# Kernel optimization log

Measured on AMD Instinct MI355X. Metric: run time of the kernel, lower is better.

The kernel has to match this reference:

```python
import jax, jax.numpy as jnp
from jax import lax
import numpy as np


def _conv3x3(x, w, b):
    # x: [B,C,H,W], w: [O,I,3,3] (OIHW), SAME padding, stride 1
    y = lax.conv_general_dilated(x, w, window_strides=(1, 1), padding='SAME',
                                 dimension_numbers=('NCHW', 'OIHW', 'NCHW'))
    return y + b[None, :, None, None]


def setup_inputs() -> dict:
    key = jax.random.key(0)
    ks = jax.random.split(key, 9)
    B, C, H, W = 4, 64, 64, 64
    wscale = 1.0 / np.sqrt(C * 9)  # keep conv outputs / attention logits sane
    x = jax.random.normal(ks[0], (B, C, H, W), dtype=jnp.float32)
    wq = jax.random.normal(ks[1], (C, C, 3, 3), dtype=jnp.float32) * wscale
    bq = jax.random.normal(ks[2], (C,), dtype=jnp.float32) * 0.1
    wk = jax.random.normal(ks[3], (C, C, 3, 3), dtype=jnp.float32) * wscale
    bk = jax.random.normal(ks[4], (C,), dtype=jnp.float32) * 0.1
    wv = jax.random.normal(ks[5], (C, C, 3, 3), dtype=jnp.float32) * wscale
    bv = jax.random.normal(ks[6], (C,), dtype=jnp.float32) * 0.1
    pos_gamma = jax.random.normal(ks[7], (1,), dtype=jnp.float32)
    chan_gamma = jax.random.normal(ks[8], (1,), dtype=jnp.float32)
    return {'x': x, 'wq': wq, 'bq': bq, 'wk': wk, 'bk': bk, 'wv': wv, 'bv': bv,
            'pos_gamma': pos_gamma, 'chan_gamma': chan_gamma}


def reference(x, wq, bq, wk, bk, wv, bv, pos_gamma, chan_gamma):
    B, C, H, W = x.shape
    N = H * W
    # position (spatial) self-attention over N = H*W locations
    q = _conv3x3(x, wq, bq).reshape(B, C, N)
    k = _conv3x3(x, wk, bk).reshape(B, C, N)
    v = _conv3x3(x, wv, bv).reshape(B, C, N)
    # attn[b,i,j] = softmax_j( sum_c q[b,c,i] * k[b,c,j] )
    pos_attn = jax.nn.softmax(jnp.einsum('bci,bcj->bij', q, k), axis=-1)
    # pos_out[b,c,j] = sum_i v[b,c,i] * attn[b,i,j]  (matches torch.bmm(v, attn))
    pos = jnp.einsum('bci,bij->bcj', v, pos_attn).reshape(B, C, H, W)
    pos_out = pos_gamma * pos + x
    # channel self-attention over C channels (x is its own q/k/v)
    xf = x.reshape(B, C, N)
    chan_attn = jax.nn.softmax(jnp.einsum('bcn,bdn->bcd', xf, xf), axis=-1)
    chan = jnp.einsum('bcd,bdn->bcn', chan_attn, xf).reshape(B, C, H, W)
    chan_out = chan_gamma * chan + x
    return pos_out + chan_out
```

## Files before the change

### kernel.cpp

```cpp
#include <hip/hip_runtime.h>

#define OFF_XV2   65536u
#define OFF_GP    589824u
#define OFF_Q2    1048576u
#define OFF_K2    2097152u
#define OFF_V2    3145728u
#define OFF_X2    3670016u
#define OFF_WT    4194304u
#define OFF_INVL  4452352u
#define OFF_A     4730880u
#define WS_FLOATS 4747264u

typedef short s8v __attribute__((ext_vector_type(8)));
typedef float f16v __attribute__((ext_vector_type(16)));

#define MFMA32(a, b, c) __builtin_amdgcn_mfma_f32_32x32x16_bf16((a), (b), (c), 0, 0, 0)

__device__ __forceinline__ unsigned short bf16_rne(float f) {
    union { float f; unsigned int u; } v; v.f = f;
    unsigned int r = v.u + 0x7FFFu + ((v.u >> 16) & 1u);
    return (unsigned short)(r >> 16);
}
__device__ __forceinline__ float bf2f(unsigned short h) {
    union { unsigned int u; float f; } t; t.u = ((unsigned int)h) << 16;
    return t.f;
}
__device__ __forceinline__ void split2(float f, unsigned short& h, unsigned short& l) {
    unsigned short hh = bf16_rne(f);
    h = hh;
    l = bf16_rne(f - bf2f(hh));
}
__device__ __forceinline__ unsigned int cvtpk(float lo, float hi) {
    unsigned int r;
    asm("v_cvt_pk_bf16_f32 %0, %1, %2" : "=v"(r) : "v"(lo), "v"(hi));
    return r;
}
__device__ __forceinline__ void pl32swap(unsigned int& a, unsigned int& b) {
    asm volatile("v_permlane32_swap_b32 %0, %1" : "+v"(a), "+v"(b));
}
__device__ __forceinline__ s8v mk8(unsigned int w0, unsigned int w1,
                                   unsigned int w2, unsigned int w3) {
    union { unsigned int u[4]; s8v v; } t;
    t.u[0] = w0; t.u[1] = w1; t.u[2] = w2; t.u[3] = w3;
    return t.v;
}
__device__ __forceinline__ f16v zero16() {
    f16v z;
#pragma unroll
    for (int i = 0; i < 16; ++i) z[i] = 0.0f;
    return z;
}


__global__ void k_wtrans(const float* __restrict__ wq, const float* __restrict__ wk,
                         const float* __restrict__ wv, unsigned short* __restrict__ wf) {
    int t = blockIdx.x * 256 + threadIdx.x;
    int f = t >> 9, pos = t & 511;
    int lane = pos >> 3, e = pos & 7;
    int oc = f & 1, kst = (f >> 1) & 3;
    int ct = f >> 3;
    int tap = ct % 9, conv = ct / 9;
    int o = oc * 32 + (lane & 31);
    int ci = kst * 16 + (lane >> 5) * 8 + e;
    const float* w = (conv == 0) ? wq : (conv == 1) ? wk : wv;
    float v = w[(o * 64 + ci) * 9 + tap];
    unsigned short hh, ll;
    split2(v, hh, ll);
    wf[(f * 2 + 0) * 512 + pos] = hh;
    wf[(f * 2 + 1) * 512 + pos] = ll;
}

__global__ __launch_bounds__(256) void k_xpack(const float* __restrict__ x,
                                               unsigned short* __restrict__ X2,
                                               unsigned short* __restrict__ XV2) {
    int gid = blockIdx.x * 256 + threadIdx.x;
    int b = gid >> 16;
    int c = (gid >> 10) & 63;
    int n4 = (gid & 1023) * 4;
    float4 v = *(const float4*)(x + (size_t)(b * 64 + c) * 4096 + n4);
    unsigned short hv[4] = {bf16_rne(v.x), bf16_rne(v.y), bf16_rne(v.z), bf16_rne(v.w)};
    int kst = c >> 4, e = c & 7, hb = (c >> 3) & 1;
#pragma unroll
    for (int u = 0; u < 4; ++u) {
        int n = n4 + u;
        int nch = n >> 5, lane = (n & 31) + 32 * hb;
        X2[(size_t)((b * 128 + nch) * 4 + kst) * 512 + lane * 8 + e] = hv[u];
    }
    int ich = n4 >> 5, ksub = (n4 >> 4) & 1, cb = c >> 5;
    int lane2 = (c & 31) + 32 * ((n4 >> 3) & 1);
    size_t xi = (size_t)(((b * 128 + ich) * 2 + ksub) * 2 + cb) * 512 + lane2 * 8 + (n4 & 7);
    unsigned long long w = (unsigned long long)hv[0]
                         | ((unsigned long long)hv[1] << 16)
                         | ((unsigned long long)hv[2] << 32)
                         | ((unsigned long long)hv[3] << 48);
    *(unsigned long long*)(XV2 + xi) = w;
}

__global__ __launch_bounds__(384) void k_conv(
        const float* __restrict__ x, const unsigned short* __restrict__ wf,
        const float* __restrict__ bq, const float* __restrict__ bk, const float* __restrict__ bv,
        unsigned short* __restrict__ Q2, unsigned short* __restrict__ K2,
        unsigned short* __restrict__ V2) {
    int nb = blockIdx.x;
    int b = blockIdx.y;
    int h = nb >> 1, w0 = (nb & 1) * 32;

    __shared__ unsigned short xwh[6528];
    __shared__ unsigned short xwl[6528];

    int tid = threadIdx.x;
    for (int idx = tid; idx < 6528; idx += 384) {
        int W = idx % 34;
        int c = (idx / 34) & 63;
        int dy = idx / (34 * 64);
        int hs = h + dy - 1, wi = w0 + W - 1;
        float v = 0.0f;
        if (hs >= 0 && hs < 64 && wi >= 0 && wi < 64)
            v = x[((b * 64 + c) * 64 + hs) * 64 + wi];
        unsigned short hh_, ll_;
        split2(v, hh_, ll_);
        int row = dy * 34 + W;
        int byt = row * 128 + c * 2;
        int swz = byt ^ ((row & 7) << 4);
        *(unsigned short*)((char*)xwh + swz) = hh_;
        *(unsigned short*)((char*)xwl + swz) = ll_;
    }
    __syncthreads();

    int lane = tid & 63, wv = tid >> 6;
    int conv = wv >> 1, oc = wv & 1;
    int hh = lane >> 5, l31 = lane & 31;

    const float* bias = (conv == 0) ? bq : (conv == 1) ? bk : bv;
    f16v D;
    if (conv < 2) {
#pragma unroll
        for (int r = 0; r < 16; ++r)
            D[r] = bias[oc * 32 + (r & 3) + 8 * (r >> 2) + 4 * hh];
    } else {
        float bvv = bias[oc * 32 + l31];
#pragma unroll
        for (int r = 0; r < 16; ++r) D[r] = bvv;
    }

#pragma unroll
    for (int tap = 0; tap < 9; ++tap) {
        int dy = tap / 3, dx = tap % 3;
#pragma unroll
        for (int kst = 0; kst < 4; ++kst) {
            int f = ((conv * 9 + tap) * 4 + kst) * 2 + oc;
            s8v Wh = *(const s8v*)(wf + (f * 2 + 0) * 512 + lane * 8);
            s8v Wl = *(const s8v*)(wf + (f * 2 + 1) * 512 + lane * 8);
            int row = dy * 34 + dx + l31;
            int byt = row * 128 + kst * 32 + hh * 16;
            int swz = byt ^ ((row & 7) << 4);
            s8v Xh = *(const s8v*)((const char*)xwh + swz);
            s8v Xl = *(const s8v*)((const char*)xwl + swz);
            if (conv < 2) {
                D = MFMA32(Wh, Xh, D);
                D = MFMA32(Wh, Xl, D);
                D = MFMA32(Wl, Xh, D);
            } else {
                D = MFMA32(Xh, Wh, D);
                D = MFMA32(Xl, Wh, D);
                D = MFMA32(Xh, Wl, D);
            }
        }
    }

    if (conv < 2) {
        unsigned short sh[16], sl[16];
#pragma unroll
        for (int r = 0; r < 16; ++r) split2(D[r], sh[r], sl[r]);
        unsigned int ah0 = sh[0] | ((unsigned int)sh[1] << 16), ah1 = sh[2] | ((unsigned int)sh[3] << 16);
        unsigned int ah2 = sh[4] | ((unsigned int)sh[5] << 16), ah3 = sh[6] | ((unsigned int)sh[7] << 16);
        pl32swap(ah0, ah2); pl32swap(ah1, ah3);
        s8v F0h = mk8(ah0, ah1, ah2, ah3);
        unsigned int al0 = sl[0] | ((unsigned int)sl[1] << 16), al1 = sl[2] | ((unsigned int)sl[3] << 16);
        unsigned int al2 = sl[4] | ((unsigned int)sl[5] << 16), al3 = sl[6] | ((unsigned int)sl[7] << 16);
        pl32swap(al0, al2); pl32swap(al1, al3);
        s8v F0l = mk8(al0, al1, al2, al3);
        unsigned int bh0 = sh[8] | ((unsigned int)sh[9] << 16), bh1 = sh[10] | ((unsigned int)sh[11] << 16);
        unsigned int bh2 = sh[12] | ((unsigned int)sh[13] << 16), bh3 = sh[14] | ((unsigned int)sh[15] << 16);
        pl32swap(bh0, bh2); pl32swap(bh1, bh3);
        s8v F1h = mk8(bh0, bh1, bh2, bh3);
        unsigned int bl0 = sl[8] | ((unsigned int)sl[9] << 16), bl1 = sl[10] | ((unsigned int)sl[11] << 16);
        unsigned int bl2 = sl[12] | ((unsigned int)sl[13] << 16), bl3 = sl[14] | ((unsigned int)sl[15] << 16);
        pl32swap(bl0, bl2); pl32swap(bl1, bl3);
        s8v F1l = mk8(bl0, bl1, bl2, bl3);
        unsigned short* dst = (conv == 0) ? Q2 : K2;
        size_t b0 = (size_t)(((b * 128 + nb) * 4 + oc * 2 + 0) * 2) * 512 + lane * 8;
        size_t b1 = (size_t)(((b * 128 + nb) * 4 + oc * 2 + 1) * 2) * 512 + lane * 8;
        *(s8v*)(dst + b0) = F0h;
        *(s8v*)(dst + b0 + 512) = F0l;
        *(s8v*)(dst + b1) = F1h;
        *(s8v*)(dst + b1 + 512) = F1l;
    } else {
        unsigned int a0 = cvtpk(D[0], D[1]),  a1 = cvtpk(D[2], D[3]);
        unsigned int a2 = cvtpk(D[4], D[5]),  a3 = cvtpk(D[6], D[7]);
        pl32swap(a0, a2); pl32swap(a1, a3);
        s8v F0h = mk8(a0, a1, a2, a3);
        unsigned int b0w = cvtpk(D[8], D[9]),  b1w = cvtpk(D[10], D[11]);
        unsigned int b2w = cvtpk(D[12], D[13]), b3w = cvtpk(D[14], D[15]);
        pl32swap(b0w, b2w); pl32swap(b1w, b3w);
        s8v F1h = mk8(b0w, b1w, b2w, b3w);
        size_t v0 = (size_t)(((b * 128 + nb) * 2 + 0) * 2 + oc) * 512 + lane * 8;
        size_t v1 = (size_t)(((b * 128 + nb) * 2 + 1) * 2 + oc) * 512 + lane * 8;
        *(s8v*)(V2 + v0) = F0h;
        *(s8v*)(V2 + v1) = F1h;
    }
}

__global__ __launch_bounds__(256) void k_gram(const unsigned short* __restrict__ XV2,
                                              float* __restrict__ Gp) {
    int kp = blockIdx.x, b = blockIdx.y;
    int tid = threadIdx.x, lane = tid & 63, wv = tid >> 6;
    int cb1 = wv & 1, cb2 = wv >> 1;
    f16v G = zero16();
#pragma unroll
    for (int t = 0; t < 8; ++t) {
        int ich = kp * 8 + t;
        const unsigned short* base = XV2 + (size_t)(b * 128 + ich) * 2048 + lane * 8;
        s8v a0 = *(const s8v*)(base + (0 * 2 + cb1) * 512);
        s8v b0 = *(const s8v*)(base + (0 * 2 + cb2) * 512);
        s8v a1 = *(const s8v*)(base + (1 * 2 + cb1) * 512);
        s8v b1 = *(const s8v*)(base + (1 * 2 + cb2) * 512);
        G = MFMA32(a0, b0, G);
        G = MFMA32(a1, b1, G);
    }
    int hh = lane >> 5, l31 = lane & 31;
#pragma unroll
    for (int r = 0; r < 16; ++r) {
        int cc = cb1 * 32 + (r & 3) + 8 * (r >> 2) + 4 * hh;
        int dd = cb2 * 32 + l31;
        Gp[(size_t)(kp * 4 + b) * 4096 + cc * 64 + dd] = G[r];
    }
}

__global__ void k_asm(const float* __restrict__ Gp, unsigned short* __restrict__ A2) {
    int row = blockIdx.x;
    int d = threadIdx.x;
    int b = row >> 6, c = row & 63;
    float g = 0.0f;
#pragma unroll
    for (int p = 0; p < 16; ++p) g += Gp[(size_t)(p * 4 + b) * 4096 + c * 64 + d];
    float mx = g;
    for (int off = 32; off >= 1; off >>= 1) mx = fmaxf(mx, __shfl_xor(mx, off, 64));
    float e = __expf(g - mx);
    float s = e;
    for (int off = 32; off >= 1; off >>= 1) s += __shfl_xor(s, off, 64);
    float a = e / s;
    int cb = c >> 5, kst = d >> 4;
    int lane2 = (c & 31) + 32 * ((d >> 3) & 1);
    A2[(size_t)((b * 2 + cb) * 4 + kst) * 512 + lane2 * 8 + (d & 7)] = bf16_rne(a);
}

__global__ __launch_bounds__(512, 2) void k_pass1(
        const unsigned short* __restrict__ Q2, const unsigned short* __restrict__ K2,
        float* __restrict__ invl) {
    int flat = blockIdx.x;
    int xcd = flat & 7;
    int b = xcd >> 1;
    int ichp = (xcd & 1) * 32 + (flat >> 3);
    int ich0 = ichp * 2;
    int tid = threadIdx.x, lane = tid & 63, wv = tid >> 6;

    __shared__ float lsum[8][2][32];

    const unsigned short* qp = Q2 + (size_t)(b * 128 + ich0) * 4096 + lane * 8;
    s8v q0f0 = *(const s8v*)(qp);
    s8v q0f1 = *(const s8v*)(qp + 512);
    s8v q0f2 = *(const s8v*)(qp + 1024);
    s8v q0f3 = *(const s8v*)(qp + 1536);
    s8v q0f4 = *(const s8v*)(qp + 2048);
    s8v q0f5 = *(const s8v*)(qp + 2560);
    s8v q0f6 = *(const s8v*)(qp + 3072);
    s8v q0f7 = *(const s8v*)(qp + 3584);
    s8v q1f0 = *(const s8v*)(qp + 4096);
    s8v q1f1 = *(const s8v*)(qp + 4608);
    s8v q1f2 = *(const s8v*)(qp + 5120);
    s8v q1f3 = *(const s8v*)(qp + 5632);
    s8v q1f4 = *(const s8v*)(qp + 6144);
    s8v q1f5 = *(const s8v*)(qp + 6656);
    s8v q1f6 = *(const s8v*)(qp + 7168);
    s8v q1f7 = *(const s8v*)(qp + 7680);

    float la0 = 0.f, la1 = 0.f, lb0 = 0.f, lb1 = 0.f;
#pragma unroll 1
    for (int t = 0; t < 16; ++t) {
        int jch = wv * 16 + t;
        const unsigned short* kp = K2 + (size_t)(b * 128 + jch) * 4096 + lane * 8;
        s8v kf0 = *(const s8v*)(kp);
        s8v kf1 = *(const s8v*)(kp + 512);
        s8v kf2 = *(const s8v*)(kp + 1024);
        s8v kf3 = *(const s8v*)(kp + 1536);
        s8v kf4 = *(const s8v*)(kp + 2048);
        s8v kf5 = *(const s8v*)(kp + 2560);
        s8v kf6 = *(const s8v*)(kp + 3072);
        s8v kf7 = *(const s8v*)(kp + 3584);
        {
            f16v Sa = zero16(), Sb = zero16();
            Sa = MFMA32(kf0, q0f0, Sa);
            Sa = MFMA32(kf0, q0f1, Sa);
            Sa = MFMA32(kf1, q0f0, Sa);
            Sa = MFMA32(kf2, q0f2, Sa);
            Sa = MFMA32(kf2, q0f3, Sa);
            Sa = MFMA32(kf3, q0f2, Sa);
            Sb = MFMA32(kf4, q0f4, Sb);
            Sb = MFMA32(kf4, q0f5, Sb);
            Sb = MFMA32(kf5, q0f4, Sb);
            Sb = MFMA32(kf6, q0f6, Sb);
            Sb = MFMA32(kf6, q0f7, Sb);
            Sb = MFMA32(kf7, q0f6, Sb);
#pragma unroll
            for (int r = 0; r < 8; ++r) la0 += __expf(Sa[r] + Sb[r]);
#pragma unroll
            for (int r = 8; r < 16; ++r) la1 += __expf(Sa[r] + Sb[r]);
        }
        {
            f16v Sa = zero16(), Sb = zero16();
            Sa = MFMA32(kf0, q1f0, Sa);
            Sa = MFMA32(kf0, q1f1, Sa);
            Sa = MFMA32(kf1, q1f0, Sa);
            Sa = MFMA32(kf2, q1f2, Sa);
            Sa = MFMA32(kf2, q1f3, Sa);
            Sa = MFMA32(kf3, q1f2, Sa);
            Sb = MFMA32(kf4, q1f4, Sb);
            Sb = MFMA32(kf4, q1f5, Sb);
            Sb = MFMA32(kf5, q1f4, Sb);
            Sb = MFMA32(kf6, q1f6, Sb);
            Sb = MFMA32(kf6, q1f7, Sb);
            Sb = MFMA32(kf7, q1f6, Sb);
#pragma unroll
            for (int r = 0; r < 8; ++r) lb0 += __expf(Sa[r] + Sb[r]);
#pragma unroll
            for (int r = 8; r < 16; ++r) lb1 += __expf(Sa[r] + Sb[r]);
        }
    }
    float lacc0 = la0 + la1;
    lacc0 += __shfl_xor(lacc0, 32);
    float lacc1 = lb0 + lb1;
    lacc1 += __shfl_xor(lacc1, 32);
    if (lane < 32) {
        lsum[wv][0][lane] = lacc0;
        lsum[wv][1][lane] = lacc1;
    }
    __syncthreads();
    if (tid < 64) {
        int ic = tid >> 5, iL = tid & 31;
        float s = 0.f;
#pragma unroll
        for (int p = 0; p < 8; ++p) s += lsum[p][ic][iL];
        invl[b * 4096 + (ich0 + ic) * 32 + iL] = 1.0f / s;
    }
}

__global__ __launch_bounds__(256) void k_vnorm(
        unsigned short* __restrict__ V2, const float* __restrict__ invl) {
    int u = blockIdx.x * 256 + threadIdx.x;
    int lane = u & 63, ksub = (u >> 7) & 1;
    int ich = (u >> 8) & 127, b = u >> 15;
    int n0 = ich * 32 + ksub * 16 + (lane >> 5) * 8;
    size_t base = (size_t)u * 8;
    s8v vh = *(s8v*)(V2 + base);
    float4 iv0 = *(const float4*)(invl + b * 4096 + n0);
    float4 iv1 = *(const float4*)(invl + b * 4096 + n0 + 4);
    float ivv[8] = {iv0.x, iv0.y, iv0.z, iv0.w, iv1.x, iv1.y, iv1.z, iv1.w};
    s8v o;
#pragma unroll
    for (int e = 0; e < 8; ++e)
        o[e] = (short)bf16_rne(bf2f((unsigned short)vh[e]) * ivv[e]);
    *(s8v*)(V2 + base) = o;
}

__global__ __launch_bounds__(512, 2) void k_pass2(
        const unsigned short* __restrict__ Q2, const unsigned short* __restrict__ K2,
        const unsigned short* __restrict__ V2, const unsigned short* __restrict__ X2,
        const unsigned short* __restrict__ A2, const float* __restrict__ x,
        const float* __restrict__ pg, const float* __restrict__ cg,
        float* __restrict__ out) {
    int flat = blockIdx.x;
    int xcd = flat & 7;
    int b = xcd >> 1;
    int jtp = (xcd & 1) * 32 + (flat >> 3);
    int jt0 = jtp * 2;
    int tid = threadIdx.x, lane = tid & 63, wv = tid >> 6;

    __shared__ float smem[12288];
    unsigned short* Klds = (unsigned short*)(smem + 8192);
    float* rl = smem;

    {
        const unsigned short* ksrc = K2 + (size_t)(b * 128 + jt0) * 4096;
#pragma unroll
        for (int s = 0; s < 2; ++s) {
            int seg = tid + s * 512;
            *(s8v*)(Klds + seg * 8) = *(const s8v*)(ksrc + seg * 8);
        }
    }
    __syncthreads();

    f16v O0a = zero16(), O1a = zero16();
    f16v O0b = zero16(), O1b = zero16();

#pragma unroll 1
    for (int t = 0; t < 16; ++t) {
        int ich = wv * 16 + t;
        const unsigned short* qp = Q2 + (size_t)(b * 128 + ich) * 4096 + lane * 8;
        s8v qf0 = *(const s8v*)(qp);
        s8v qf1 = *(const s8v*)(qp + 512);
        s8v qf2 = *(const s8v*)(qp + 1024);
        s8v qf3 = *(const s8v*)(qp + 1536);
        s8v qf4 = *(const s8v*)(qp + 2048);
        s8v qf5 = *(const s8v*)(qp + 2560);
        s8v qf6 = *(const s8v*)(qp + 3072);
        s8v qf7 = *(const s8v*)(qp + 3584);
        const unsigned short* vp = V2 + (size_t)(b * 128 + ich) * 2048 + lane * 8;
        s8v vA = *(const s8v*)(vp);
        s8v vB = *(const s8v*)(vp + 512);
        s8v vC = *(const s8v*)(vp + 1024);
        s8v vD = *(const s8v*)(vp + 1536);

#pragma unroll
        for (int js = 0; js < 2; ++js) {
            const unsigned short* kl = Klds + js * 4096 + lane * 8;
            s8v kf0 = *(const s8v*)(kl);
            s8v kf1 = *(const s8v*)(kl + 512);
            s8v kf2 = *(const s8v*)(kl + 1024);
            s8v kf3 = *(const s8v*)(kl + 1536);
            s8v kf4 = *(const s8v*)(kl + 2048);
            s8v kf5 = *(const s8v*)(kl + 2560);
            s8v kf6 = *(const s8v*)(kl + 3072);
            s8v kf7 = *(const s8v*)(kl + 3584);

            f16v Sa = zero16(), Sb = zero16();
            Sa = MFMA32(qf0, kf0, Sa);
            Sa = MFMA32(qf0, kf1, Sa);
            Sa = MFMA32(qf1, kf0, Sa);
            Sa = MFMA32(qf2, kf2, Sa);
            Sa = MFMA32(qf2, kf3, Sa);
            Sa = MFMA32(qf3, kf2, Sa);
            Sb = MFMA32(qf4, kf4, Sb);
            Sb = MFMA32(qf4, kf5, Sb);
            Sb = MFMA32(qf5, kf4, Sb);
            Sb = MFMA32(qf6, kf6, Sb);
            Sb = MFMA32(qf6, kf7, Sb);
            Sb = MFMA32(qf7, kf6, Sb);

            float p[16];
#pragma unroll
            for (int r = 0; r < 16; ++r) p[r] = __expf(Sa[r] + Sb[r]);

            unsigned int a0 = cvtpk(p[0], p[1]),  a1 = cvtpk(p[2], p[3]);
            unsigned int a2 = cvtpk(p[4], p[5]),  a3 = cvtpk(p[6], p[7]);
            pl32swap(a0, a2);
            pl32swap(a1, a3);
            s8v P0 = mk8(a0, a1, a2, a3);
            unsigned int b0 = cvtpk(p[8], p[9]),  b1 = cvtpk(p[10], p[11]);
            unsigned int b2 = cvtpk(p[12], p[13]), b3 = cvtpk(p[14], p[15]);
            pl32swap(b0, b2);
            pl32swap(b1, b3);
            s8v P1 = mk8(b0, b1, b2, b3);

            if (js == 0) {
                O0a = MFMA32(vA, P0, O0a);
                O0a = MFMA32(vC, P1, O0a);
                O1a = MFMA32(vB, P0, O1a);
                O1a = MFMA32(vD, P1, O1a);
            } else {
                O0b = MFMA32(vA, P0, O0b);
                O0b = MFMA32(vC, P1, O0b);
                O1b = MFMA32(vB, P0, O1b);
                O1b = MFMA32(vD, P1, O1b);
            }
        }
    }

    int hh = lane >> 5, jj = lane & 31;
    float s0[4], s1[4];
    if (wv < 4) {
#pragma unroll
        for (int r = 0; r < 16; ++r) {
            int c = (r & 3) + 8 * (r >> 2) + 4 * hh;
            rl[(wv * 64 + c) * 32 + jj] = O0a[r];
            rl[(wv * 64 + c + 32) * 32 + jj] = O1a[r];
        }
    }
    __syncthreads();
#pragma unroll
    for (int k = 0; k < 4; ++k) {
        int el = tid + k * 512;
        s0[k] = ((rl[el] + rl[2048 + el]) + rl[4096 + el]) + rl[6144 + el];
    }
    __syncthreads();
    if (wv >= 4) {
#pragma unroll
        for (int r = 0; r < 16; ++r) {
            int c = (r & 3) + 8 * (r >> 2) + 4 * hh;
            rl[((wv - 4) * 64 + c) * 32 + jj] = O0a[r];
            rl[((wv - 4) * 64 + c + 32) * 32 + jj] = O1a[r];
        }
    }
    __syncthreads();
#pragma unroll
    for (int k = 0; k < 4; ++k) {
        int el = tid + k * 512;
        s0[k] = ((s0[k] + rl[el]) + rl[2048 + el]) + rl[4096 + el];
        s0[k] += rl[6144 + el];
    }
    __syncthreads();
    if (wv < 4) {
#pragma unroll
        for (int r = 0; r < 16; ++r) {
            int c = (r & 3) + 8 * (r >> 2) + 4 * hh;
            rl[(wv * 64 + c) * 32 + jj] = O0b[r];
            rl[(wv * 64 + c + 32) * 32 + jj] = O1b[r];
        }
    }
    __syncthreads();
#pragma unroll
    for (int k = 0; k < 4; ++k) {
        int el = tid + k * 512;
        s1[k] = ((rl[el] + rl[2048 + el]) + rl[4096 + el]) + rl[6144 + el];
    }
    __syncthreads();
    if (wv >= 4) {
#pragma unroll
        for (int r = 0; r < 16; ++r) {
            int c = (r & 3) + 8 * (r >> 2) + 4 * hh;
            rl[((wv - 4) * 64 + c) * 32 + jj] = O0b[r];
            rl[((wv - 4) * 64 + c + 32) * 32 + jj] = O1b[r];
        }
    }
    __syncthreads();
#pragma unroll
    for (int k = 0; k < 4; ++k) {
        int el = tid + k * 512;
        s1[k] = ((s1[k] + rl[el]) + rl[2048 + el]) + rl[4096 + el];
        s1[k] += rl[6144 + el];
    }
    __syncthreads();

    float* chan = smem;
    float* xres = smem + 4160;
    if (wv < 4) {
        int jts = wv >> 1, cb = wv & 1;
        f16v Dc = zero16();
#pragma unroll
        for (int kst = 0; kst < 4; ++kst) {
            s8v af = *(const s8v*)(A2 + (size_t)((b * 2 + cb) * 4 + kst) * 512 + lane * 8);
            s8v xf = *(const s8v*)(X2 + (size_t)((b * 128 + jt0 + jts) * 4 + kst) * 512 + lane * 8);
            Dc = MFMA32(af, xf, Dc);
        }
#pragma unroll
        for (int r = 0; r < 16; ++r) {
            int c = cb * 32 + (r & 3) + 8 * (r >> 2) + 4 * hh;
            chan[c * 65 + jts * 32 + jj] = Dc[r];
        }
    }
#pragma unroll
    for (int k = 0; k < 8; ++k) {
        int el = tid + k * 512;
        int c = el >> 6, j2 = el & 63;
        xres[el] = x[(size_t)(b * 64 + c) * 4096 + jtp * 64 + j2];
    }
    __syncthreads();
    float pgv = pg[0], cgv = cg[0];
#pragma unroll
    for (int k = 0; k < 4; ++k) {
        int el = tid + k * 512;
        int c = el >> 5, j2 = el & 31;
        size_t ob = (size_t)(b * 64 + c) * 4096 + jtp * 64;
        out[ob + j2] = pgv * s0[k] + cgv * chan[c * 65 + j2] + 2.0f * xres[c * 64 + j2];
        out[ob + 32 + j2] = pgv * s1[k] + cgv * chan[c * 65 + 32 + j2] + 2.0f * xres[c * 64 + 32 + j2];
    }
}

extern "C" void kernel_launch(void* const* d_in, const int* in_sizes, int n_in,
                              void* d_out, int out_size, void* d_ws, size_t ws_size,
                              hipStream_t stream) {
    const float* x  = (const float*)d_in[0];
    const float* wq = (const float*)d_in[1];
    const float* bq = (const float*)d_in[2];
    const float* wk = (const float*)d_in[3];
    const float* bk = (const float*)d_in[4];
    const float* wv = (const float*)d_in[5];
    const float* bv = (const float*)d_in[6];
    const float* pg = (const float*)d_in[7];
    const float* cg = (const float*)d_in[8];
    float* out = (float*)d_out;

    if (ws_size < (size_t)WS_FLOATS * sizeof(float)) return;
    float* ws = (float*)d_ws;
    unsigned short* XV2 = (unsigned short*)(ws + OFF_XV2);
    float* Gp = ws + OFF_GP;
    unsigned short* Q2  = (unsigned short*)(ws + OFF_Q2);
    unsigned short* K2  = (unsigned short*)(ws + OFF_K2);
    unsigned short* V2  = (unsigned short*)(ws + OFF_V2);
    unsigned short* X2  = (unsigned short*)(ws + OFF_X2);
    unsigned short* wfb = (unsigned short*)(ws + OFF_WT);
    float* invl = ws + OFF_INVL;
    unsigned short* A2  = (unsigned short*)(ws + OFF_A);

    k_wtrans<<<432, 256, 0, stream>>>(wq, wk, wv, wfb);
    k_xpack<<<1024, 256, 0, stream>>>(x, X2, XV2);
    k_conv<<<dim3(128, 4), 384, 0, stream>>>(x, wfb, bq, bk, bv, Q2, K2, V2);
    k_gram<<<dim3(16, 4), 256, 0, stream>>>(XV2, Gp);
    k_asm<<<256, 64, 0, stream>>>(Gp, A2);
    k_pass1<<<256, 512, 0, stream>>>(Q2, K2, invl);
    k_vnorm<<<512, 256, 0, stream>>>(V2, invl);
    k_pass2<<<256, 512, 0, stream>>>(Q2, K2, V2, X2, A2, x, pg, cg, out);
}
```

Baseline: 110.2 us.

## Split attention passes over key/query halves and move epilogue to final kernel

The two attention passes now split the reduction dimension in half, launching twice as many blocks (512) so more CUs are occupied. Partial row sums and partial outputs go to workspace and are combined in the normalization kernel and in a new final kernel, which also does the channel-attention MFMA and the residual. The two small prep kernels are merged into one launch. In exchange there is extra global traffic for the partial results and one more kernel launch.

```diff
diff --git a/kernel.cpp b/kernel.cpp
--- a/kernel.cpp
+++ b/kernel.cpp
@@ -1,5 +1,7 @@
 #include <hip/hip_runtime.h>
 
+#define OFF_LP    0u
+#define OFF_OP1   0u
 #define OFF_XV2   65536u
 #define OFF_GP    589824u
 #define OFF_Q2    1048576u
@@ -7,7 +9,6 @@
 #define OFF_V2    3145728u
 #define OFF_X2    3670016u
 #define OFF_WT    4194304u
-#define OFF_INVL  4452352u
 #define OFF_A     4730880u
 #define WS_FLOATS 4747264u
 
@@ -52,48 +53,50 @@
 }
 
 
-__global__ void k_wtrans(const float* __restrict__ wq, const float* __restrict__ wk,
-                         const float* __restrict__ wv, unsigned short* __restrict__ wf) {
-    int t = blockIdx.x * 256 + threadIdx.x;
-    int f = t >> 9, pos = t & 511;
-    int lane = pos >> 3, e = pos & 7;
-    int oc = f & 1, kst = (f >> 1) & 3;
-    int ct = f >> 3;
-    int tap = ct % 9, conv = ct / 9;
-    int o = oc * 32 + (lane & 31);
-    int ci = kst * 16 + (lane >> 5) * 8 + e;
-    const float* w = (conv == 0) ? wq : (conv == 1) ? wk : wv;
-    float v = w[(o * 64 + ci) * 9 + tap];
-    unsigned short hh, ll;
-    split2(v, hh, ll);
-    wf[(f * 2 + 0) * 512 + pos] = hh;
-    wf[(f * 2 + 1) * 512 + pos] = ll;
-}
-
-__global__ __launch_bounds__(256) void k_xpack(const float* __restrict__ x,
-                                               unsigned short* __restrict__ X2,
-                                               unsigned short* __restrict__ XV2) {
-    int gid = blockIdx.x * 256 + threadIdx.x;
-    int b = gid >> 16;
-    int c = (gid >> 10) & 63;
-    int n4 = (gid & 1023) * 4;
-    float4 v = *(const float4*)(x + (size_t)(b * 64 + c) * 4096 + n4);
-    unsigned short hv[4] = {bf16_rne(v.x), bf16_rne(v.y), bf16_rne(v.z), bf16_rne(v.w)};
-    int kst = c >> 4, e = c & 7, hb = (c >> 3) & 1;
-#pragma unroll
-    for (int u = 0; u < 4; ++u) {
-        int n = n4 + u;
-        int nch = n >> 5, lane = (n & 31) + 32 * hb;
-        X2[(size_t)((b * 128 + nch) * 4 + kst) * 512 + lane * 8 + e] = hv[u];
-    }
-    int ich = n4 >> 5, ksub = (n4 >> 4) & 1, cb = c >> 5;
-    int lane2 = (c & 31) + 32 * ((n4 >> 3) & 1);
-    size_t xi = (size_t)(((b * 128 + ich) * 2 + ksub) * 2 + cb) * 512 + lane2 * 8 + (n4 & 7);
-    unsigned long long w = (unsigned long long)hv[0]
-                         | ((unsigned long long)hv[1] << 16)
-                         | ((unsigned long long)hv[2] << 32)
-                         | ((unsigned long long)hv[3] << 48);
-    *(unsigned long long*)(XV2 + xi) = w;
+__global__ __launch_bounds__(256) void k_prep(
+        const float* __restrict__ wq, const float* __restrict__ wk,
+        const float* __restrict__ wv, const float* __restrict__ x,
+        unsigned short* __restrict__ wf, unsigned short* __restrict__ X2,
+        unsigned short* __restrict__ XV2) {
+    int bid = blockIdx.x, tid = threadIdx.x;
+    if (bid < 432) {
+        int t = bid * 256 + tid;
+        int f = t >> 9, pos = t & 511;
+        int lane = pos >> 3, e = pos & 7;
+        int oc = f & 1, kst = (f >> 1) & 3;
+        int ct = f >> 3;
+        int tap = ct % 9, conv = ct / 9;
+        int o = oc * 32 + (lane & 31);
+        int ci = kst * 16 + (lane >> 5) * 8 + e;
+        const float* w = (conv == 0) ? wq : (conv == 1) ? wk : wv;
+        float v = w[(o * 64 + ci) * 9 + tap];
+        unsigned short hh, ll;
+        split2(v, hh, ll);
+        wf[(f * 2 + 0) * 512 + pos] = hh;
+        wf[(f * 2 + 1) * 512 + pos] = ll;
+    } else {
+        int gid = (bid - 432) * 256 + tid;
+        int b = gid >> 16;
+        int c = (gid >> 10) & 63;
+        int n4 = (gid & 1023) * 4;
+        float4 v = *(const float4*)(x + (size_t)(b * 64 + c) * 4096 + n4);
+        unsigned short hv[4] = {bf16_rne(v.x), bf16_rne(v.y), bf16_rne(v.z), bf16_rne(v.w)};
+        int kst = c >> 4, e = c & 7, hb = (c >> 3) & 1;
+#pragma unroll
+        for (int u = 0; u < 4; ++u) {
+            int n = n4 + u;
+            int nch = n >> 5, lane = (n & 31) + 32 * hb;
+            X2[(size_t)((b * 128 + nch) * 4 + kst) * 512 + lane * 8 + e] = hv[u];
+        }
+        int ich = n4 >> 5, ksub = (n4 >> 4) & 1, cb = c >> 5;
+        int lane2 = (c & 31) + 32 * ((n4 >> 3) & 1);
+        size_t xi = (size_t)(((b * 128 + ich) * 2 + ksub) * 2 + cb) * 512 + lane2 * 8 + (n4 & 7);
+        unsigned long long w = (unsigned long long)hv[0]
+                             | ((unsigned long long)hv[1] << 16)
+                             | ((unsigned long long)hv[2] << 32)
+                             | ((unsigned long long)hv[3] << 48);
+        *(unsigned long long*)(XV2 + xi) = w;
+    }
 }
 
 __global__ __launch_bounds__(384) void k_conv(
@@ -257,11 +260,12 @@
 
 __global__ __launch_bounds__(512, 2) void k_pass1(
         const unsigned short* __restrict__ Q2, const unsigned short* __restrict__ K2,
-        float* __restrict__ invl) {
+        float* __restrict__ lpart) {
     int flat = blockIdx.x;
     int xcd = flat & 7;
     int b = xcd >> 1;
-    int ichp = (xcd & 1) * 32 + (flat >> 3);
+    int rest = (xcd & 1) * 64 + (flat >> 3);
+    int ichp = rest & 63, jh = rest >> 6;
     int ich0 = ichp * 2;
     int tid = threadIdx.x, lane = tid & 63, wv = tid >> 6;
 
@@ -287,8 +291,8 @@
 
     float la0 = 0.f, la1 = 0.f, lb0 = 0.f, lb1 = 0.f;
 #pragma unroll 1
-    for (int t = 0; t < 16; ++t) {
-        int jch = wv * 16 + t;
+    for (int t = 0; t < 8; ++t) {
+        int jch = jh * 64 + wv * 8 + t;
         const unsigned short* kp = K2 + (size_t)(b * 128 + jch) * 4096 + lane * 8;
         s8v kf0 = *(const s8v*)(kp);
         s8v kf1 = *(const s8v*)(kp + 512);
@@ -351,38 +355,43 @@
         float s = 0.f;
 #pragma unroll
         for (int p = 0; p < 8; ++p) s += lsum[p][ic][iL];
-        invl[b * 4096 + (ich0 + ic) * 32 + iL] = 1.0f / s;
-    }
-}
-
-__global__ __launch_bounds__(256) void k_vnorm(
-        unsigned short* __restrict__ V2, const float* __restrict__ invl) {
+        lpart[jh * 16384 + b * 4096 + (ich0 + ic) * 32 + iL] = s;
+    }
+}
+
+__global__ __launch_bounds__(256) void k_mvn(
+        unsigned short* __restrict__ V2, const float* __restrict__ lpart) {
     int u = blockIdx.x * 256 + threadIdx.x;
     int lane = u & 63, ksub = (u >> 7) & 1;
     int ich = (u >> 8) & 127, b = u >> 15;
     int n0 = ich * 32 + ksub * 16 + (lane >> 5) * 8;
     size_t base = (size_t)u * 8;
     s8v vh = *(s8v*)(V2 + base);
-    float4 iv0 = *(const float4*)(invl + b * 4096 + n0);
-    float4 iv1 = *(const float4*)(invl + b * 4096 + n0 + 4);
-    float ivv[8] = {iv0.x, iv0.y, iv0.z, iv0.w, iv1.x, iv1.y, iv1.z, iv1.w};
+    const float* l0 = lpart + b * 4096 + n0;
+    float4 a0 = *(const float4*)(l0);
+    float4 a1 = *(const float4*)(l0 + 4);
+    float4 c0 = *(const float4*)(l0 + 16384);
+    float4 c1 = *(const float4*)(l0 + 16384 + 4);
+    float lv[8] = {a0.x + c0.x, a0.y + c0.y, a0.z + c0.z, a0.w + c0.w,
+                   a1.x + c1.x, a1.y + c1.y, a1.z + c1.z, a1.w + c1.w};
     s8v o;
 #pragma unroll
-    for (int e = 0; e < 8; ++e)
-        o[e] = (short)bf16_rne(bf2f((unsigned short)vh[e]) * ivv[e]);
+    for (int e = 0; e < 8; ++e) {
+        float inv = 1.0f / lv[e];
+        o[e] = (short)bf16_rne(bf2f((unsigned short)vh[e]) * inv);
+    }
     *(s8v*)(V2 + base) = o;
 }
 
 __global__ __launch_bounds__(512, 2) void k_pass2(
         const unsigned short* __restrict__ Q2, const unsigned short* __restrict__ K2,
-        const unsigned short* __restrict__ V2, const unsigned short* __restrict__ X2,
-        const unsigned short* __restrict__ A2, const float* __restrict__ x,
-        const float* __restrict__ pg, const float* __restrict__ cg,
-        float* __restrict__ out) {
+        const unsigned short* __restrict__ V2, float* __restrict__ outp,
+        float* __restrict__ op1) {
     int flat = blockIdx.x;
     int xcd = flat & 7;
     int b = xcd >> 1;
-    int jtp = (xcd & 1) * 32 + (flat >> 3);
+    int rest = (xcd & 1) * 64 + (flat >> 3);
+    int jtp = rest & 63, ih = rest >> 6;
     int jt0 = jtp * 2;
     int tid = threadIdx.x, lane = tid & 63, wv = tid >> 6;
 
@@ -404,8 +413,8 @@
     f16v O0b = zero16(), O1b = zero16();
 
 #pragma unroll 1
-    for (int t = 0; t < 16; ++t) {
-        int ich = wv * 16 + t;
+    for (int t = 0; t < 8; ++t) {
+        int ich = ih * 64 + wv * 8 + t;
         const unsigned short* qp = Q2 + (size_t)(b * 128 + ich) * 4096 + lane * 8;
         s8v qf0 = *(const s8v*)(qp);
         s8v qf1 = *(const s8v*)(qp + 512);
@@ -539,11 +548,34 @@
         s1[k] = ((s1[k] + rl[el]) + rl[2048 + el]) + rl[4096 + el];
         s1[k] += rl[6144 + el];
     }
-    __syncthreads();
-
-    float* chan = smem;
-    float* xres = smem + 4160;
-    if (wv < 4) {
+
+    float* dst = ih ? op1 : outp;
+#pragma unroll
+    for (int k = 0; k < 4; ++k) {
+        int el = tid + k * 512;
+        int c = el >> 5, j2 = el & 31;
+        size_t ob = (size_t)(b * 64 + c) * 4096 + jtp * 64;
+        dst[ob + j2] = s0[k];
+        dst[ob + 32 + j2] = s1[k];
+    }
+}
+
+__global__ __launch_bounds__(256) void k_final(
+        const float* __restrict__ op1, const unsigned short* __restrict__ X2,
+        const unsigned short* __restrict__ A2, const float* __restrict__ x,
+        const float* __restrict__ pg, const float* __restrict__ cg,
+        float* __restrict__ out) {
+    int flat = blockIdx.x;
+    int xcd = flat & 7;
+    int b = xcd >> 1;
+    int jtp = (xcd & 1) * 32 + (flat >> 3);
+    int jt0 = jtp * 2;
+    int tid = threadIdx.x, lane = tid & 63, wv = tid >> 6;
+    int hh = lane >> 5, jj = lane & 31;
+
+    __shared__ float chan[64 * 65];
+
+    {
         int jts = wv >> 1, cb = wv & 1;
         f16v Dc = zero16();
 #pragma unroll
@@ -558,21 +590,15 @@
             chan[c * 65 + jts * 32 + jj] = Dc[r];
         }
     }
-#pragma unroll
-    for (int k = 0; k < 8; ++k) {
-        int el = tid + k * 512;
+    __syncthreads();
+    float pgv = pg[0], cgv = cg[0];
+#pragma unroll
+    for (int k = 0; k < 16; ++k) {
+        int el = tid + k * 256;
         int c = el >> 6, j2 = el & 63;
-        xres[el] = x[(size_t)(b * 64 + c) * 4096 + jtp * 64 + j2];
-    }
-    __syncthreads();
-    float pgv = pg[0], cgv = cg[0];
-#pragma unroll
-    for (int k = 0; k < 4; ++k) {
-        int el = tid + k * 512;
-        int c = el >> 5, j2 = el & 31;
-        size_t ob = (size_t)(b * 64 + c) * 4096 + jtp * 64;
-        out[ob + j2] = pgv * s0[k] + cgv * chan[c * 65 + j2] + 2.0f * xres[c * 64 + j2];
-        out[ob + 32 + j2] = pgv * s1[k] + cgv * chan[c * 65 + 32 + j2] + 2.0f * xres[c * 64 + 32 + j2];
+        size_t loc = (size_t)(b * 64 + c) * 4096 + jtp * 64 + j2;
+        float pos = out[loc] + op1[loc];
+        out[loc] = pgv * pos + cgv * chan[c * 65 + j2] + 2.0f * x[loc];
     }
 }
 
@@ -592,6 +618,8 @@
 
     if (ws_size < (size_t)WS_FLOATS * sizeof(float)) return;
     float* ws = (float*)d_ws;
+    float* lpart = ws + OFF_LP;
+    float* op1   = ws + OFF_OP1;
     unsigned short* XV2 = (unsigned short*)(ws + OFF_XV2);
     float* Gp = ws + OFF_GP;
     unsigned short* Q2  = (unsigned short*)(ws + OFF_Q2);
@@ -599,15 +627,14 @@
     unsigned short* V2  = (unsigned short*)(ws + OFF_V2);
     unsigned short* X2  = (unsigned short*)(ws + OFF_X2);
     unsigned short* wfb = (unsigned short*)(ws + OFF_WT);
-    float* invl = ws + OFF_INVL;
     unsigned short* A2  = (unsigned short*)(ws + OFF_A);
 
-    k_wtrans<<<432, 256, 0, stream>>>(wq, wk, wv, wfb);
-    k_xpack<<<1024, 256, 0, stream>>>(x, X2, XV2);
+    k_prep<<<1456, 256, 0, stream>>>(wq, wk, wv, x, wfb, X2, XV2);
     k_conv<<<dim3(128, 4), 384, 0, stream>>>(x, wfb, bq, bk, bv, Q2, K2, V2);
     k_gram<<<dim3(16, 4), 256, 0, stream>>>(XV2, Gp);
     k_asm<<<256, 64, 0, stream>>>(Gp, A2);
-    k_pass1<<<256, 512, 0, stream>>>(Q2, K2, invl);
-    k_vnorm<<<512, 256, 0, stream>>>(V2, invl);
-    k_pass2<<<256, 512, 0, stream>>>(Q2, K2, V2, X2, A2, x, pg, cg, out);
-}
+    k_pass1<<<512, 512, 0, stream>>>(Q2, K2, lpart);
+    k_mvn<<<512, 256, 0, stream>>>(V2, lpart);
+    k_pass2<<<512, 512, 0, stream>>>(Q2, K2, V2, out, op1);
+    k_final<<<256, 256, 0, stream>>>(op1, X2, A2, x, pg, cg, out);
+}
```

After: 115.8 us. +5.1%, slower.
